# Kernel optimization log

Measured on AMD Instinct MI355X. Metric: run time of the kernel, lower is better.

## Reference

```python
import jax, jax.numpy as jnp
import numpy as np

EMBED_DIMS = 1024
NUM_HEADS = 16
HEAD_DIMS = EMBED_DIMS // NUM_HEADS


def setup_inputs() -> dict:
    key = jax.random.key(0)
    k_x, k_wqkv, k_bqkv, k_wp, k_bp = jax.random.split(key, 5)
    B, N, D = 2, 2048, EMBED_DIMS
    x = jax.random.normal(k_x, (B, N, D), dtype=jnp.float32)
    # torch nn.Linear(in, out): weight [out, in], y = x @ W.T + b
    s = 1.0 / np.sqrt(D)
    W_qkv = jax.random.uniform(k_wqkv, (3 * D, D), jnp.float32, -s, s)
    b_qkv = jax.random.uniform(k_bqkv, (3 * D,), jnp.float32, -s, s)
    W_proj = jax.random.uniform(k_wp, (D, D), jnp.float32, -s, s)
    b_proj = jax.random.uniform(k_bp, (D,), jnp.float32, -s, s)
    return {"x": x, "W_qkv": W_qkv, "b_qkv": b_qkv, "W_proj": W_proj, "b_proj": b_proj}


def reference(x, W_qkv, b_qkv, W_proj, b_proj):
    B, N, D = x.shape
    H, Hd = NUM_HEADS, HEAD_DIMS
    # qkv projection: [B, N, 3, H, Hd] -> split q, k, v as [B, H, N, Hd]
    qkv = (x @ W_qkv.T + b_qkv).reshape(B, N, 3, H, Hd).transpose(2, 0, 3, 1, 4)
    q, k, v = qkv[0], qkv[1], qkv[2]
    scale = 1.0 / jnp.sqrt(jnp.asarray(Hd, x.dtype))
    attn = jnp.einsum("bhqd,bhkd->bhqk", q, k) * scale  # [B, H, N, N]
    attn = jax.nn.softmax(attn, axis=-1)
    out = jnp.einsum("bhqk,bhkd->bhqd", attn, v)  # [B, H, N, Hd]
    out = out.transpose(0, 2, 1, 3).reshape(B, N, D)
    out = out @ W_proj.T + b_proj
    return out
```

## Files before the change

kernel.cpp:

```cpp
#include <hip/hip_runtime.h>

typedef _Float16 f16x8 __attribute__((ext_vector_type(8)));
typedef __attribute__((ext_vector_type(4))) float f32x4;

static __device__ __forceinline__ unsigned short f2h(float f) {
  return __builtin_bit_cast(unsigned short, (_Float16)f);
}

static __device__ __forceinline__ unsigned int pk2(float a, float b) {
  return (unsigned int)f2h(a) | ((unsigned int)f2h(b) << 16);
}

#if __has_builtin(__builtin_amdgcn_exp2f)
#define EXP2(x) __builtin_amdgcn_exp2f(x)
#else
#define EXP2(x) exp2f(x)
#endif

#define GLOAD_LDS16(gp, lp)                                          \
  __builtin_amdgcn_global_load_lds(                                  \
      (const __attribute__((address_space(1))) unsigned int*)(gp),   \
      (__attribute__((address_space(3))) unsigned int*)(lp), 16, 0, 0)

__global__ __launch_bounds__(256) void cvt_all(
    const float* __restrict__ X, const float* __restrict__ Wq,
    const float* __restrict__ Wp, unsigned short* __restrict__ Xb,
    unsigned short* __restrict__ Wqb, unsigned short* __restrict__ Wpb) {
  const int i = blockIdx.x * 256 + threadIdx.x;
  const float4* src;
  unsigned short* dst;
  int off;
  if (i < 1048576) {
    src = (const float4*)X; dst = Xb; off = i;
  } else if (i < 1835008) {
    src = (const float4*)Wq; dst = Wqb; off = i - 1048576;
  } else {
    src = (const float4*)Wp; dst = Wpb; off = i - 1835008;
  }
  const float4 v = src[off];
  *(ushort4*)(dst + (size_t)off * 4) =
      make_ushort4(f2h(v.x), f2h(v.y), f2h(v.z), f2h(v.w));
}

__global__ __launch_bounds__(256, 3) void qkv_gemm(
    const unsigned short* __restrict__ Xb, const unsigned short* __restrict__ Wb,
    const float* __restrict__ bias, unsigned short* __restrict__ Qb,
    unsigned short* __restrict__ Kb, unsigned short* __restrict__ Vt) {
  __shared__ __align__(16) unsigned short A_sh[2][128 * 32];
  __shared__ __align__(16) unsigned short B_sh[2][128 * 32];
  const int n0 = blockIdx.x * 128, m0 = blockIdx.y * 128;
  const int tid = threadIdx.x, lane = tid & 63, wave = tid >> 6;
  const int wr = wave >> 1, wc = wave & 1;
  const int lm = lane & 15, lg = lane >> 4;
  const int r4 = lane >> 2;
  const int sg8 = (((lane & 3) ^ ((r4 >> 1) & 3)) * 8);
  const int lgx = (lg ^ ((lm >> 1) & 3)) * 8;

  f32x4 acc[4][4] = {};

#define QSTAGE(k0_, b_)                                                       \
  do {                                                                        \
    _Pragma("unroll")                                                         \
    for (int j = 0; j < 2; ++j) {                                             \
      const int chunk = wave * 2 + j;                                         \
      const int row = chunk * 16 + r4;                                        \
      GLOAD_LDS16(Xb + (size_t)(m0 + row) * 1024 + (k0_) + sg8,               \
                  &A_sh[b_][chunk * 512]);                                    \
      GLOAD_LDS16(Wb + (size_t)(n0 + row) * 1024 + (k0_) + sg8,               \
                  &B_sh[b_][chunk * 512]);                                    \
    }                                                                         \
  } while (0)

  QSTAGE(0, 0);

  for (int it = 0; it < 32; ++it) {
    const int cur = it & 1;
    __syncthreads();
    if (it < 31) QSTAGE((it + 1) * 32, cur ^ 1);

    f16x8 af[4], bfr[4];
#pragma unroll
    for (int mi = 0; mi < 4; ++mi)
      af[mi] = *(const f16x8*)&A_sh[cur][(wr * 64 + mi * 16 + lm) * 32 + lgx];
#pragma unroll
    for (int ni = 0; ni < 4; ++ni)
      bfr[ni] = *(const f16x8*)&B_sh[cur][(wc * 64 + ni * 16 + lm) * 32 + lgx];
    __builtin_amdgcn_s_setprio(1);
#pragma unroll
    for (int mi = 0; mi < 4; ++mi)
#pragma unroll
      for (int ni = 0; ni < 4; ++ni)
        acc[mi][ni] = __builtin_amdgcn_mfma_f32_16x16x32_f16(
            af[mi], bfr[ni], acc[mi][ni], 0, 0, 0);
    __builtin_amdgcn_s_setprio(0);
  }
#undef QSTAGE

  const float qscale = 0.18033688011112042f;
#pragma unroll
  for (int mi = 0; mi < 4; ++mi) {
#pragma unroll
    for (int ni = 0; ni < 4; ++ni) {
      const int gn = n0 + wc * 64 + ni * 16 + lm;
      const float bv = bias[gn];
      const int which = gn >> 10;
      const int h = (gn >> 6) & 15;
      const int hd = gn & 63;
      float v[4];
#pragma unroll
      for (int r = 0; r < 4; ++r) v[r] = acc[mi][ni][r] + bv;
      const int gm0 = m0 + wr * 64 + mi * 16 + lg * 4;
      const int bb = gm0 >> 11;
      const int nq0 = gm0 & 2047;
      if (which == 0) {
        unsigned short* p = Qb + (((size_t)bb * 16 + h) * 2048 + nq0) * 64 + hd;
        p[0] = f2h(v[0] * qscale);   p[64] = f2h(v[1] * qscale);
        p[128] = f2h(v[2] * qscale); p[192] = f2h(v[3] * qscale);
      } else if (which == 1) {
        unsigned short* p = Kb + (((size_t)bb * 16 + h) * 2048 + nq0) * 64 + hd;
        p[0] = f2h(v[0]);   p[64] = f2h(v[1]);
        p[128] = f2h(v[2]); p[192] = f2h(v[3]);
      } else {
        *(ushort4*)(Vt + (((size_t)bb * 16 + h) * 64 + hd) * 2048 + nq0) =
            make_ushort4(f2h(v[0]), f2h(v[1]), f2h(v[2]), f2h(v[3]));
      }
    }
  }
}

__global__ __launch_bounds__(512, 4) void attn_kernel(
    const unsigned short* __restrict__ Qb, const unsigned short* __restrict__ Kb,
    const unsigned short* __restrict__ Vt, unsigned short* __restrict__ Ob) {
  __shared__ __align__(16) unsigned short K_sh[2][2][64 * 32];
  __shared__ __align__(16) unsigned short V_sh[2][2][64 * 32];
  const int bh = blockIdx.y, q0 = blockIdx.x * 128;
  const size_t base = (size_t)bh * (2048 * 64);
  const unsigned short* Qp = Qb + base;
  const unsigned short* Kp = Kb + base;
  const unsigned short* Vp = Vt + base;
  const int tid = threadIdx.x, lane = tid & 63, wave = tid >> 6;
  const int lm = lane & 15, lg = lane >> 4;
  const int r4 = lane >> 2;
  const int sg8 = (((lane & 3) ^ ((r4 >> 1) & 3)) * 8);
  const int lgx = (lg ^ ((lm >> 1) & 3)) * 8;

  f16x8 qf[2];
#pragma unroll
  for (int kc = 0; kc < 2; ++kc)
    qf[kc] = *(const f16x8*)(Qp +
        (size_t)(q0 + wave * 16 + lm) * 64 + kc * 32 + lg * 8);

  f32x4 o[4] = {};
  float lsum = 0.0f;

  const bool isV = wave >= 4;
  const int plane = wave & 1;
  const int half = (wave >> 1) & 1;

#define STAGE(kt_, b_)                                                        \
  do {                                                                        \
    if (!isV) {                                                               \
      _Pragma("unroll")                                                       \
      for (int qv = 0; qv < 2; ++qv)                                          \
        GLOAD_LDS16(Kp + (size_t)((kt_) * 64 + half * 32 + qv * 16 + r4) * 64 \
                        + plane * 32 + sg8,                                   \
                    &K_sh[b_][plane][(half * 2 + qv) * 512]);                 \
    } else {                                                                  \
      _Pragma("unroll")                                                       \
      for (int qv = 0; qv < 2; ++qv)                                          \
        GLOAD_LDS16(Vp + (size_t)(half * 32 + qv * 16 + r4) * 2048 +          \
                        (kt_) * 64 + plane * 32 + sg8,                        \
                    &V_sh[b_][plane][(half * 2 + qv) * 512]);                 \
    }                                                                         \
  } while (0)

  STAGE(0, 0);

  for (int kt = 0; kt < 32; ++kt) {
    const int cur = kt & 1;
    __syncthreads();
    if (kt < 31) STAGE(kt + 1, cur ^ 1);

    f32x4 s[4] = {};
#pragma unroll
    for (int kc = 0; kc < 2; ++kc) {
#pragma unroll
      for (int ni = 0; ni < 4; ++ni) {
        const f16x8 kf =
            *(const f16x8*)&K_sh[cur][kc][(ni * 16 + lm) * 32 + lgx];
        s[ni] = __builtin_amdgcn_mfma_f32_16x16x32_f16(kf, qf[kc], s[ni], 0, 0, 0);
      }
    }

    unsigned int Wp_[4][2];
#pragma unroll
    for (int ni = 0; ni < 4; ++ni) {
      const float p0 = EXP2(s[ni][0]), p1 = EXP2(s[ni][1]);
      const float p2 = EXP2(s[ni][2]), p3 = EXP2(s[ni][3]);
      lsum += (p0 + p1) + (p2 + p3);
      Wp_[ni][0] = pk2(p0, p1);
      Wp_[ni][1] = pk2(p2, p3);
    }

#pragma unroll
    for (int kc = 0; kc < 2; ++kc) {
      auto t0 = __builtin_amdgcn_permlane32_swap(Wp_[2 * kc][0], Wp_[2 * kc + 1][0],
                                                 false, false);
      auto u0 = __builtin_amdgcn_permlane16_swap(t0[0], t0[1], false, false);
      auto t1 = __builtin_amdgcn_permlane32_swap(Wp_[2 * kc][1], Wp_[2 * kc + 1][1],
                                                 false, false);
      auto u1 = __builtin_amdgcn_permlane16_swap(t1[0], t1[1], false, false);
      union { unsigned int u[4]; f16x8 v; } pa;
      pa.u[0] = u0[0];
      pa.u[1] = u1[0];
      pa.u[2] = u0[1];
      pa.u[3] = u1[1];
#pragma unroll
      for (int ni = 0; ni < 4; ++ni) {
        const f16x8 vb =
            *(const f16x8*)&V_sh[cur][kc][(ni * 16 + lm) * 32 + lgx];
        o[ni] = __builtin_amdgcn_mfma_f32_16x16x32_f16(pa.v, vb, o[ni], 0, 0, 0);
      }
    }
  }
#undef STAGE

  float total = lsum;
  total += __shfl_xor(total, 16);
  total += __shfl_xor(total, 32);

  const int b = bh >> 4, h = bh & 15;
#pragma unroll
  for (int r = 0; r < 4; ++r) {
    const float inv = 1.0f / __shfl(total, (lane & 48) | (lg * 4 + r));
    const int nq = q0 + wave * 16 + lg * 4 + r;
    unsigned short* p = Ob + ((size_t)(b * 2048 + nq) * 16 + h) * 64 + lm;
    p[0] = f2h(o[0][r] * inv);
    p[16] = f2h(o[1][r] * inv);
    p[32] = f2h(o[2][r] * inv);
    p[48] = f2h(o[3][r] * inv);
  }
}

__global__ __launch_bounds__(256) void proj_gemm(
    const unsigned short* __restrict__ A, const unsigned short* __restrict__ Wb,
    const float* __restrict__ bias, float* __restrict__ Out) {
  __shared__ __align__(16) unsigned short A_sh[2][64 * 32];
  __shared__ __align__(16) unsigned short B_sh[2][128 * 32];
  const int n0 = blockIdx.x * 128, m0 = blockIdx.y * 64;
  const int tid = threadIdx.x, lane = tid & 63, wave = tid >> 6;
  const int wr = wave >> 1, wc = wave & 1, lm = lane & 15, lg = lane >> 4;
  const int r4 = lane >> 2;
  const int sg8 = (((lane & 3) ^ ((r4 >> 1) & 3)) * 8);
  const int lgx = (lg ^ ((lm >> 1) & 3)) * 8;

  f32x4 acc[2][4] = {};

#define PSTAGE(k0_, b_)                                                       \
  do {                                                                        \
    {                                                                         \
      const int row = wave * 16 + r4;                                         \
      GLOAD_LDS16(A + (size_t)(m0 + row) * 1024 + (k0_) + sg8,                \
                  &A_sh[b_][wave * 512]);                                     \
    }                                                                         \
    _Pragma("unroll")                                                         \
    for (int j = 0; j < 2; ++j) {                                             \
      const int chunk = wave * 2 + j;                                         \
      const int row = chunk * 16 + r4;                                        \
      GLOAD_LDS16(Wb + (size_t)(n0 + row) * 1024 + (k0_) + sg8,               \
                  &B_sh[b_][chunk * 512]);                                    \
    }                                                                         \
  } while (0)

  PSTAGE(0, 0);

  for (int it = 0; it < 32; ++it) {
    const int cur = it & 1;
    __syncthreads();
    if (it < 31) PSTAGE((it + 1) * 32, cur ^ 1);

    f16x8 af[2], bfr[4];
#pragma unroll
    for (int mi = 0; mi < 2; ++mi)
      af[mi] = *(const f16x8*)&A_sh[cur][(wr * 32 + mi * 16 + lm) * 32 + lgx];
#pragma unroll
    for (int ni = 0; ni < 4; ++ni)
      bfr[ni] = *(const f16x8*)&B_sh[cur][(wc * 64 + ni * 16 + lm) * 32 + lgx];
#pragma unroll
    for (int mi = 0; mi < 2; ++mi)
#pragma unroll
      for (int ni = 0; ni < 4; ++ni)
        acc[mi][ni] = __builtin_amdgcn_mfma_f32_16x16x32_f16(
            af[mi], bfr[ni], acc[mi][ni], 0, 0, 0);
  }
#undef PSTAGE

#pragma unroll
  for (int mi = 0; mi < 2; ++mi)
#pragma unroll
    for (int ni = 0; ni < 4; ++ni) {
      const int gn = n0 + wc * 64 + ni * 16 + lm;
      const float bv = bias[gn];
#pragma unroll
      for (int r = 0; r < 4; ++r) {
        const int gm = m0 + wr * 32 + mi * 16 + lg * 4 + r;
        Out[(size_t)gm * 1024 + gn] = acc[mi][ni][r] + bv;
      }
    }
}

extern "C" void kernel_launch(void* const* d_in, const int* in_sizes, int n_in,
                              void* d_out, int out_size, void* d_ws, size_t ws_size,
                              hipStream_t stream) {
  const float* x      = (const float*)d_in[0];
  const float* W_qkv  = (const float*)d_in[1];
  const float* b_qkv  = (const float*)d_in[2];
  const float* W_proj = (const float*)d_in[3];
  const float* b_proj = (const float*)d_in[4];
  float* out = (float*)d_out;

  unsigned short* Qb  = (unsigned short*)d_ws;
  unsigned short* Kb  = Qb + 4194304;
  unsigned short* Vt  = Kb + 4194304;
  unsigned short* Ao  = Vt + 4194304;
  unsigned short* Xb  = Ao + 4194304;
  unsigned short* Wqb = Xb + 4194304;
  unsigned short* Wpb = Wqb + 3145728;

  cvt_all<<<8192, 256, 0, stream>>>(x, W_qkv, W_proj, Xb, Wqb, Wpb);
  qkv_gemm<<<dim3(24, 32), 256, 0, stream>>>(Xb, Wqb, b_qkv, Qb, Kb, Vt);
  attn_kernel<<<dim3(16, 32), 512, 0, stream>>>(Qb, Kb, Vt, Ao);
  proj_gemm<<<dim3(8, 64), 256, 0, stream>>>(Ao, Wpb, b_proj, out);
}
```

Measured before the change: 193.0 us.

## Split attention waves across key halves with two query tiles per wave

Each attention wave now handles 32 query rows and one half of each 64-key tile, instead of 16 rows over the full tile. Each K and V fragment read from LDS then feeds two MFMAs. After the loop, the partial outputs and row sums are reduced across wave pairs through extra shared memory. The aim is to cut LDS fragment reads per MFMA, at the cost of more accumulator registers, extra LDS, and an end-of-kernel reduction that can lower occupancy.

```diff
diff --git a/kernel.cpp b/kernel.cpp
--- a/kernel.cpp
+++ b/kernel.cpp
@@ -133,6 +133,8 @@
     const unsigned short* __restrict__ Vt, unsigned short* __restrict__ Ob) {
   __shared__ __align__(16) unsigned short K_sh[2][2][64 * 32];
   __shared__ __align__(16) unsigned short V_sh[2][2][64 * 32];
+  __shared__ __align__(16) f32x4 Om[4][4][64];
+  __shared__ float Ls2[4][64];
   const int bh = blockIdx.y, q0 = blockIdx.x * 128;
   const size_t base = (size_t)bh * (2048 * 64);
   const unsigned short* Qp = Qb + base;
@@ -144,14 +146,19 @@
   const int sg8 = (((lane & 3) ^ ((r4 >> 1) & 3)) * 8);
   const int lgx = (lg ^ ((lm >> 1) & 3)) * 8;
 
-  f16x8 qf[2];
-#pragma unroll
-  for (int kc = 0; kc < 2; ++kc)
-    qf[kc] = *(const f16x8*)(Qp +
-        (size_t)(q0 + wave * 16 + lm) * 64 + kc * 32 + lg * 8);
-
-  f32x4 o[4] = {};
-  float lsum = 0.0f;
+  const int qg = wave >> 1;
+  const int khalf = wave & 1;
+
+  f16x8 qf[2][2];
+#pragma unroll
+  for (int mi = 0; mi < 2; ++mi)
+#pragma unroll
+    for (int kc = 0; kc < 2; ++kc)
+      qf[mi][kc] = *(const f16x8*)(Qp +
+          (size_t)(q0 + qg * 32 + mi * 16 + lm) * 64 + kc * 32 + lg * 8);
+
+  f32x4 o[2][4] = {};
+  float lsum[2] = {0.0f, 0.0f};
 
   const bool isV = wave >= 4;
   const int plane = wave & 1;
@@ -181,33 +188,43 @@
     __syncthreads();
     if (kt < 31) STAGE(kt + 1, cur ^ 1);
 
-    f32x4 s[4] = {};
+    f32x4 s[2][2] = {};
 #pragma unroll
     for (int kc = 0; kc < 2; ++kc) {
 #pragma unroll
-      for (int ni = 0; ni < 4; ++ni) {
-        const f16x8 kf =
-            *(const f16x8*)&K_sh[cur][kc][(ni * 16 + lm) * 32 + lgx];
-        s[ni] = __builtin_amdgcn_mfma_f32_16x16x32_f16(kf, qf[kc], s[ni], 0, 0, 0);
-      }
-    }
-
-    unsigned int Wp_[4][2];
-#pragma unroll
-    for (int ni = 0; ni < 4; ++ni) {
-      const float p0 = EXP2(s[ni][0]), p1 = EXP2(s[ni][1]);
-      const float p2 = EXP2(s[ni][2]), p3 = EXP2(s[ni][3]);
-      lsum += (p0 + p1) + (p2 + p3);
-      Wp_[ni][0] = pk2(p0, p1);
-      Wp_[ni][1] = pk2(p2, p3);
-    }
-
-#pragma unroll
-    for (int kc = 0; kc < 2; ++kc) {
-      auto t0 = __builtin_amdgcn_permlane32_swap(Wp_[2 * kc][0], Wp_[2 * kc + 1][0],
+      for (int ni = 0; ni < 2; ++ni) {
+        const f16x8 kf = *(const f16x8*)
+            &K_sh[cur][kc][(khalf * 32 + ni * 16 + lm) * 32 + lgx];
+        s[0][ni] = __builtin_amdgcn_mfma_f32_16x16x32_f16(
+            kf, qf[0][kc], s[0][ni], 0, 0, 0);
+        s[1][ni] = __builtin_amdgcn_mfma_f32_16x16x32_f16(
+            kf, qf[1][kc], s[1][ni], 0, 0, 0);
+      }
+    }
+
+    unsigned int Wp_[2][2][2];
+#pragma unroll
+    for (int mi = 0; mi < 2; ++mi)
+#pragma unroll
+      for (int ni = 0; ni < 2; ++ni) {
+        const float p0 = EXP2(s[mi][ni][0]), p1 = EXP2(s[mi][ni][1]);
+        const float p2 = EXP2(s[mi][ni][2]), p3 = EXP2(s[mi][ni][3]);
+        lsum[mi] += (p0 + p1) + (p2 + p3);
+        Wp_[mi][ni][0] = pk2(p0, p1);
+        Wp_[mi][ni][1] = pk2(p2, p3);
+      }
+
+    f16x8 vb[4];
+#pragma unroll
+    for (int ni = 0; ni < 4; ++ni)
+      vb[ni] = *(const f16x8*)&V_sh[cur][khalf][(ni * 16 + lm) * 32 + lgx];
+
+#pragma unroll
+    for (int mi = 0; mi < 2; ++mi) {
+      auto t0 = __builtin_amdgcn_permlane32_swap(Wp_[mi][0][0], Wp_[mi][1][0],
                                                  false, false);
       auto u0 = __builtin_amdgcn_permlane16_swap(t0[0], t0[1], false, false);
-      auto t1 = __builtin_amdgcn_permlane32_swap(Wp_[2 * kc][1], Wp_[2 * kc + 1][1],
+      auto t1 = __builtin_amdgcn_permlane32_swap(Wp_[mi][0][1], Wp_[mi][1][1],
                                                  false, false);
       auto u1 = __builtin_amdgcn_permlane16_swap(t1[0], t1[1], false, false);
       union { unsigned int u[4]; f16x8 v; } pa;
@@ -216,29 +233,44 @@
       pa.u[2] = u0[1];
       pa.u[3] = u1[1];
 #pragma unroll
+      for (int ni = 0; ni < 4; ++ni)
+        o[mi][ni] = __builtin_amdgcn_mfma_f32_16x16x32_f16(
+            pa.v, vb[ni], o[mi][ni], 0, 0, 0);
+    }
+  }
+#undef STAGE
+
+  const int b = bh >> 4, h = bh & 15;
+#pragma unroll
+  for (int mi = 0; mi < 2; ++mi) {
+    __syncthreads();
+    if (khalf == 1) {
+#pragma unroll
+      for (int ni = 0; ni < 4; ++ni) Om[qg][ni][lane] = o[mi][ni];
+      Ls2[qg][lane] = lsum[mi];
+    }
+    __syncthreads();
+    if (khalf == 0) {
+#pragma unroll
       for (int ni = 0; ni < 4; ++ni) {
-        const f16x8 vb =
-            *(const f16x8*)&V_sh[cur][kc][(ni * 16 + lm) * 32 + lgx];
-        o[ni] = __builtin_amdgcn_mfma_f32_16x16x32_f16(pa.v, vb, o[ni], 0, 0, 0);
-      }
-    }
-  }
-#undef STAGE
-
-  float total = lsum;
-  total += __shfl_xor(total, 16);
-  total += __shfl_xor(total, 32);
-
-  const int b = bh >> 4, h = bh & 15;
-#pragma unroll
-  for (int r = 0; r < 4; ++r) {
-    const float inv = 1.0f / __shfl(total, (lane & 48) | (lg * 4 + r));
-    const int nq = q0 + wave * 16 + lg * 4 + r;
-    unsigned short* p = Ob + ((size_t)(b * 2048 + nq) * 16 + h) * 64 + lm;
-    p[0] = f2h(o[0][r] * inv);
-    p[16] = f2h(o[1][r] * inv);
-    p[32] = f2h(o[2][r] * inv);
-    p[48] = f2h(o[3][r] * inv);
+        const f32x4 t = Om[qg][ni][lane];
+        o[mi][ni][0] += t[0]; o[mi][ni][1] += t[1];
+        o[mi][ni][2] += t[2]; o[mi][ni][3] += t[3];
+      }
+      float total = lsum[mi] + Ls2[qg][lane];
+      total += __shfl_xor(total, 16);
+      total += __shfl_xor(total, 32);
+#pragma unroll
+      for (int r = 0; r < 4; ++r) {
+        const float inv = 1.0f / __shfl(total, (lane & 48) | (lg * 4 + r));
+        const int nq = q0 + qg * 32 + mi * 16 + lg * 4 + r;
+        unsigned short* p = Ob + ((size_t)(b * 2048 + nq) * 16 + h) * 64 + lm;
+        p[0] = f2h(o[mi][0][r] * inv);
+        p[16] = f2h(o[mi][1][r] * inv);
+        p[32] = f2h(o[mi][2][r] * inv);
+        p[48] = f2h(o[mi][3][r] * inv);
+      }
+    }
   }
 }
 
```

Result: faster. 186.2 us (-3.5%).
